# Performance work log

Hardware: AMD Instinct MI355X
Metric: run time of the kernel (lower is better)

Reference implementation:

```python
import jax, jax.numpy as jnp
import numpy as np

B, N, D = 4, 2048, 1024
H = 16
HD = D // H          # 64
SCALE = 1.0 / HD     # module uses 1/head_dim (NOT 1/sqrt)
NEG = -10000.0       # masked_fill value used by the module
THETA = 10000.0


def setup_inputs() -> dict:
    key = jax.random.key(0)
    ks = jax.random.split(key, 6)
    s = (1.0 / D) ** 0.5  # init_method_normal((1/dim)**0.5)
    return {
        "x": jax.random.normal(ks[0], (B, N, D), jnp.float32),
        "Wq": jax.random.normal(ks[1], (D, D), jnp.float32) * s,
        "Wk": jax.random.normal(ks[2], (D, D), jnp.float32) * s,
        "Wv": jax.random.normal(ks[3], (D, D), jnp.float32) * s,
        "Wo": jax.random.normal(ks[4], (D, D), jnp.float32) * s,
        "bo": jnp.zeros((D,), jnp.float32),
    }


def _rope(t):
    # t: [b, h, n, d]; interleaved-pair rotary (lucidrains rotate_queries_or_keys)
    d, n = t.shape[-1], t.shape[-2]
    inv_freq = 1.0 / (THETA ** (jnp.arange(0, d, 2, dtype=jnp.float32) / d))  # [d/2]
    ang = jnp.arange(n, dtype=jnp.float32)[:, None] * inv_freq[None, :]        # [n, d/2]
    cos = jnp.repeat(jnp.cos(ang), 2, axis=-1)  # [n, d]
    sin = jnp.repeat(jnp.sin(ang), 2, axis=-1)
    x1, x2 = t[..., ::2], t[..., 1::2]
    rot = jnp.stack([-x2, x1], axis=-1).reshape(t.shape)  # rotate_half
    return t * cos + rot * sin


def reference(x, Wq, Wk, Wv, Wo, bo):
    b, n, _ = x.shape
    # QKV projections (no bias; torch Linear: x @ W.T)
    q = (x @ Wq.T).reshape(b, n, H, HD).transpose(0, 2, 1, 3)  # [b,h,n,d]
    k = (x @ Wk.T).reshape(b, n, H, HD).transpose(0, 2, 1, 3)
    v = (x @ Wv.T).reshape(b, n, H, HD).transpose(0, 2, 1, 3)
    # RoPE on q, k
    q = _rope(q)
    k = _rope(k)
    # additive mask: 0 on/below diagonal, -10000 above (causal_mask=True path)
    i = jnp.arange(n)
    add_mask = jnp.where(i[:, None] >= i[None, :], 0.0, NEG).astype(x.dtype)  # [n,n]
    scores = jnp.einsum("bhqd,bhkd->bhqk", q, k) * SCALE + add_mask
    attn = jax.nn.softmax(scores, axis=-1)
    out = jnp.einsum("bhqk,bhkd->bhqd", attn, v)            # [b,h,n,d]
    out = out.transpose(0, 2, 1, 3).reshape(b, n, H * HD)    # [b,n,D]
    return out @ Wo.T + bo
```

## Files before the change

kernel.cpp:

```cpp
#include <hip/hip_runtime.h>
#include <hip/hip_bf16.h>
#include <math.h>

#define B_ 4
#define N_ 2048
#define D_ 1024
#define H_ 16
#define HD_ 64
#define SCALE_ 0.015625f
#define MD_ ((size_t)B_ * N_ * D_)
#define DD_ ((size_t)D_ * D_)
#define BHSZ_ ((size_t)N_ * HD_)
#define QSC_ 0.0225421143f

typedef __hip_bfloat16 bf16;
typedef __attribute__((ext_vector_type(8))) __bf16 bf16x8;
typedef __attribute__((ext_vector_type(4))) float f32x4;
typedef __attribute__((ext_vector_type(16))) float f32x16;

__device__ __forceinline__ float b2f(bf16 x) { return __bfloat162float(x); }
__device__ __forceinline__ bf16 f2b(float x) { return __float2bfloat16(x); }

__device__ __forceinline__ unsigned int pk2(float a, float b) {
  union { bf16 h[2]; unsigned int u; } t;
  t.h[0] = f2b(a); t.h[1] = f2b(b);
  return t.u;
}
__device__ __forceinline__ unsigned int pk2t(float a, float b) {
  return (__float_as_uint(a) >> 16) | (__float_as_uint(b) & 0xffff0000u);
}

__device__ __forceinline__ void gl_lds16(const bf16* g, bf16* l) {
  __builtin_amdgcn_global_load_lds(
      (const __attribute__((address_space(1))) void*)g,
      (__attribute__((address_space(3))) void*)l, 16, 0, 0);
}

__global__ __launch_bounds__(256) void cvt_all(
    const float* __restrict__ x,  const float* __restrict__ wq,
    const float* __restrict__ wk, const float* __restrict__ wv,
    const float* __restrict__ wo, bf16* __restrict__ xb,
    bf16* __restrict__ wb, float2* __restrict__ rt)
{
  const int blk = blockIdx.x;
  if (blk >= 6144) {
    const float LN_THETA = 9.210340371976184f;
    int e = ((blk - 6144) * 256 + (int)threadIdx.x) * 4;
    float fn = (float)(e >> 5);
#pragma unroll
    for (int p = 0; p < 4; ++p) {
      int i = (e & 31) + p;
      float inv = __expf(-((float)(2 * i) / (float)HD_) * LN_THETA);
      float sv, cv;
      sincosf(fn * inv, &sv, &cv);
      rt[e + p] = make_float2(cv, sv);
    }
    return;
  }
  const float* s; bf16* d; int i;
  if (blk < 4096)      { s = x;  d = xb;           i = blk; }
  else if (blk < 4608) { s = wq; d = wb;           i = blk - 4096; }
  else if (blk < 5120) { s = wk; d = wb + DD_;     i = blk - 4608; }
  else if (blk < 5632) { s = wv; d = wb + 2 * DD_; i = blk - 5120; }
  else                 { s = wo; d = wb + 3 * DD_; i = blk - 5632; }
  int e = (i * 256 + threadIdx.x) * 8;
  float4 a = *reinterpret_cast<const float4*>(s + e);
  float4 b = *reinterpret_cast<const float4*>(s + e + 4);
  bf16 t[8] = {f2b(a.x), f2b(a.y), f2b(a.z), f2b(a.w),
               f2b(b.x), f2b(b.y), f2b(b.z), f2b(b.w)};
  *reinterpret_cast<int4*>(d + e) = *reinterpret_cast<const int4*>(t);
}

template <int MODE>
__global__ __launch_bounds__(256) void mgemm(
    const bf16* __restrict__ A, const bf16* __restrict__ W,
    const float* __restrict__ bias, void* __restrict__ Cv,
    const float2* __restrict__ rt, int M, int N, int K)
{
  __shared__ bf16 As[128 * 32];
  __shared__ bf16 Ws[128 * 32];

  const int tid  = threadIdx.x;
  const int w    = tid >> 6;
  const int lane = tid & 63;
  const int bm   = blockIdx.y * 128;
  const int bn   = blockIdx.x * 128;

  const int wr = (w >> 1) * 64;
  const int wc = (w & 1) * 64;
  const int lm   = lane & 15;
  const int quad = lane >> 4;

  const int srow = lane >> 2;
  const int sslot = (lane & 3) ^ ((lane >> 3) & 3);
  const int scol = sslot * 8;

  const int rsw  = (quad ^ ((lm >> 1) & 3)) * 8;

  f32x4 acc[4][4] = {};

  for (int k0 = 0; k0 < K; k0 += 32) {
#pragma unroll
    for (int cc = 0; cc < 2; ++cc) {
      int c = w * 2 + cc;
      int r = c * 16 + srow;
      gl_lds16(A + (size_t)(bm + r) * K + k0 + scol, &As[c * 512]);
      gl_lds16(W + (size_t)(bn + r) * K + k0 + scol, &Ws[c * 512]);
    }
    __syncthreads();

    bf16x8 af[4], bf_[4];
#pragma unroll
    for (int mi = 0; mi < 4; ++mi)
      af[mi] = *reinterpret_cast<const bf16x8*>(&As[(wr + mi * 16 + lm) * 32 + rsw]);
#pragma unroll
    for (int ni = 0; ni < 4; ++ni)
      bf_[ni] = *reinterpret_cast<const bf16x8*>(&Ws[(wc + ni * 16 + lm) * 32 + rsw]);

#pragma unroll
    for (int mi = 0; mi < 4; ++mi)
#pragma unroll
      for (int ni = 0; ni < 4; ++ni)
        acc[mi][ni] = __builtin_amdgcn_mfma_f32_16x16x32_bf16(
            af[mi], bf_[ni], acc[mi][ni], 0, 0, 0);
    __syncthreads();
  }

#pragma unroll
  for (int mi = 0; mi < 4; ++mi) {
#pragma unroll
    for (int r = 0; r < 4; ++r) {
      int row = bm + wr + mi * 16 + quad * 4 + r;
#pragma unroll
      for (int ni = 0; ni < 4; ++ni) {
        int col = bn + wc + ni * 16 + lm;
        float v = acc[mi][ni][r];
        if (MODE == 1) {
          v += bias[col];
          reinterpret_cast<float*>(Cv)[(size_t)row * N + col] = v;
        } else {
          int reg = col >> 10;
          int cc  = col & 1023;
          int bb  = row >> 11;
          int n   = row & (N_ - 1);
          int hh  = cc >> 6;
          int dd  = cc & 63;
          float po = __shfl_xor(v, 1);
          if (reg < 2) {
            float2 cs = rt[(n << 5) + (dd >> 1)];
            v = (dd & 1) ? (v * cs.x + po * cs.y)
                         : (v * cs.x - po * cs.y);
            if (reg == 0) v *= QSC_;
            int t32 = n >> 5, m = n & 31;
            int s = dd >> 4, hb = (dd >> 3) & 1, j = dd & 7;
            reinterpret_cast<bf16*>(Cv)[(size_t)reg * MD_ +
                (size_t)(bb * H_ + hh) * BHSZ_ +
                (size_t)t32 * 2048 + s * 512 + hb * 256 + m * 8 + j] = f2b(v);
          } else {
            int t32 = n >> 5, kk = n & 31;
            int hf = kk >> 4, hb = (kk >> 3) & 1, j = kk & 7;
            reinterpret_cast<bf16*>(Cv)[2 * MD_ +
                (size_t)(bb * H_ + hh) * BHSZ_ +
                (size_t)t32 * 2048 + hf * 1024 + hb * 512 + dd * 8 + j] = f2b(v);
          }
        }
      }
    }
  }
}

__global__ __launch_bounds__(128) void fattn4_kernel(
    const bf16* __restrict__ Qf, const bf16* __restrict__ Kf,
    const bf16* __restrict__ Vf, bf16* __restrict__ O)
{
  __shared__ float Ls[32 * 64];
  __shared__ float Ll[64];

  const int wv   = threadIdx.x >> 6;
  const int lane = threadIdx.x & 63;
  const int blk  = blockIdx.x;
  const int xcd  = blk & 7;
  const int j    = blk >> 3;
  const int qt   = 63 - (j >> 3);
  const int bh   = xcd * 8 + (j & 7);
  const int b    = bh >> 4;
  const int h    = bh & 15;
  const int col  = lane & 31;
  const int hi   = lane >> 5;

  const bf16* Qb = Qf + (size_t)bh * BHSZ_ + (size_t)qt * 2048 + hi * 256 + col * 8;
  const bf16* Kb = Kf + (size_t)bh * BHSZ_ + hi * 256 + col * 8;
  const bf16* Vb = Vf + (size_t)bh * BHSZ_ + hi * 512 + col * 8;

  bf16x8 qb[4];
#pragma unroll
  for (int s = 0; s < 4; ++s)
    qb[s] = *reinterpret_cast<const bf16x8*>(Qb + s * 512);

  f32x16 o0 = {}, o1 = {};
  float lsum = 0.f;

  for (int kst = wv; kst <= qt; kst += 2) {
    const bf16* kp = Kb + (size_t)kst * 2048;
    f32x16 st = {};
#pragma unroll
    for (int s = 0; s < 4; ++s) {
      bf16x8 ka = *reinterpret_cast<const bf16x8*>(kp + s * 512);
      st = __builtin_amdgcn_mfma_f32_32x32x16_bf16(ka, qb[s], st, 0, 0, 0);
    }

    float pe[16];
    if (kst == qt) {
#pragma unroll
      for (int r = 0; r < 16; ++r) {
        int koff = (r & 3) + 8 * (r >> 2) + 4 * hi;
        float e = (koff <= col) ? exp2f(st[r]) : 0.f;
        pe[r] = e; lsum += e;
      }
    } else {
#pragma unroll
      for (int r = 0; r < 16; ++r) {
        float e = exp2f(st[r]);
        pe[r] = e; lsum += e;
      }
    }

    const bf16* vp = Vb + (size_t)kst * 2048;
#pragma unroll
    for (int hf = 0; hf < 2; ++hf) {
      unsigned int a0 = pk2t(pe[8 * hf + 0], pe[8 * hf + 1]);
      unsigned int a1 = pk2t(pe[8 * hf + 2], pe[8 * hf + 3]);
      unsigned int b0 = pk2t(pe[8 * hf + 4], pe[8 * hf + 5]);
      unsigned int b1 = pk2t(pe[8 * hf + 6], pe[8 * hf + 7]);
      unsigned int s0 = hi ? a0 : b0;
      unsigned int s1 = hi ? a1 : b1;
      unsigned int r0 = (unsigned int)__shfl_xor((int)s0, 32);
      unsigned int r1 = (unsigned int)__shfl_xor((int)s1, 32);
      union { uint4 u; bf16x8 v; } pb;
      pb.u.x = hi ? r0 : a0;
      pb.u.y = hi ? r1 : a1;
      pb.u.z = hi ? b0 : r0;
      pb.u.w = hi ? b1 : r1;

      bf16x8 v0 = *reinterpret_cast<const bf16x8*>(vp + hf * 1024);
      bf16x8 v1 = *reinterpret_cast<const bf16x8*>(vp + hf * 1024 + 256);
      o0 = __builtin_amdgcn_mfma_f32_32x32x16_bf16(v0, pb.v, o0, 0, 0, 0);
      o1 = __builtin_amdgcn_mfma_f32_32x32x16_bf16(v1, pb.v, o1, 0, 0, 0);
    }
  }

  if (wv == 1) {
#pragma unroll
    for (int r = 0; r < 16; ++r) {
      Ls[r * 64 + lane]        = o0[r];
      Ls[(16 + r) * 64 + lane] = o1[r];
    }
    Ll[lane] = lsum;
  }
  __syncthreads();
  if (wv == 0) {
    float lt = lsum + Ll[lane];
    lt += __shfl_xor(lt, 32);
    float inv = 1.f / lt;
#pragma unroll
    for (int r = 0; r < 16; ++r) {
      o0[r] = (o0[r] + Ls[r * 64 + lane]) * inv;
      o1[r] = (o1[r] + Ls[(16 + r) * 64 + lane]) * inv;
    }
    bf16* Op = O + ((size_t)(b * N_ + 32 * qt + col)) * D_ + h * HD_;
#pragma unroll
    for (int g = 0; g < 4; ++g) {
      uint2 u;
      u.x = pk2(o0[4 * g + 0], o0[4 * g + 1]);
      u.y = pk2(o0[4 * g + 2], o0[4 * g + 3]);
      *reinterpret_cast<uint2*>(Op + 8 * g + 4 * hi) = u;
      u.x = pk2(o1[4 * g + 0], o1[4 * g + 1]);
      u.y = pk2(o1[4 * g + 2], o1[4 * g + 3]);
      *reinterpret_cast<uint2*>(Op + 32 + 8 * g + 4 * hi) = u;
    }
  }
}

extern "C" void kernel_launch(void* const* d_in, const int* in_sizes, int n_in,
                              void* d_out, int out_size, void* d_ws, size_t ws_size,
                              hipStream_t stream)
{
  const float* x  = (const float*)d_in[0];
  const float* Wq = (const float*)d_in[1];
  const float* Wk = (const float*)d_in[2];
  const float* Wv = (const float*)d_in[3];
  const float* Wo = (const float*)d_in[4];
  const float* bo = (const float*)d_in[5];
  float* out = (float*)d_out;

  const int M = B_ * N_;

  bf16* xb  = (bf16*)d_ws;
  bf16* qf  = xb + MD_;
  bf16* kf  = qf + MD_;
  bf16* vf  = kf + MD_;
  bf16* Wqb = vf + MD_;
  bf16* Wob = Wqb + 3 * DD_;
  float2* rt = (float2*)(Wqb + 4 * DD_);
  bf16* ao  = xb;

  cvt_all<<<6208, 256, 0, stream>>>(x, Wq, Wk, Wv, Wo, xb, Wqb, rt);

  mgemm<0><<<dim3(24, 64), 256, 0, stream>>>(xb, Wqb, nullptr, qf, rt, M, 3 * D_, D_);

  fattn4_kernel<<<4096, 128, 0, stream>>>(qf, kf, vf, ao);

  mgemm<1><<<dim3(8, 64), 256, 0, stream>>>(ao, Wob, bo, out, nullptr, M, D_, D_);
}
```

Before: 277.3 us.

## Replace QKV GEMM with 256x256-tile, 8-wave, double-buffered pipelined kernel

The fused QKV projection moves to a new kernel using 256x256 output tiles, 512 threads and a double-buffered LDS pipeline. Global-to-LDS loads for future k-steps are interleaved with MFMA phases using explicit barriers, waitcnt and setprio. Blocks are remapped so neighbouring tiles land on the same XCD, which should improve cache reuse. The aim is to hide load latency and cut LDS traffic per FLOP, at the cost of much higher register and LDS pressure and fragile hand-tuned waitcnt counts.

```diff
diff --git a/kernel.cpp b/kernel.cpp
--- a/kernel.cpp
+++ b/kernel.cpp
@@ -35,6 +35,14 @@
       (const __attribute__((address_space(1))) void*)g,
       (__attribute__((address_space(3))) void*)l, 16, 0, 0);
 }
+
+__device__ __forceinline__ void fbar() {
+  asm volatile("" ::: "memory");
+  __builtin_amdgcn_s_barrier();
+  asm volatile("" ::: "memory");
+}
+
+#define MFMA16(a, b, c) __builtin_amdgcn_mfma_f32_16x16x32_bf16((a), (b), (c), 0, 0, 0)
 
 __global__ __launch_bounds__(256) void cvt_all(
     const float* __restrict__ x,  const float* __restrict__ wq,
@@ -71,11 +79,152 @@
   *reinterpret_cast<int4*>(d + e) = *reinterpret_cast<const int4*>(t);
 }
 
-template <int MODE>
-__global__ __launch_bounds__(256) void mgemm(
+__global__ __launch_bounds__(512, 2) void qkv8(
     const bf16* __restrict__ A, const bf16* __restrict__ W,
-    const float* __restrict__ bias, void* __restrict__ Cv,
-    const float2* __restrict__ rt, int M, int N, int K)
+    bf16* __restrict__ Cv, const float2* __restrict__ rt)
+{
+  __shared__ bf16 As[2 * 2 * 16 * 512];
+  __shared__ bf16 Bs[2 * 2 * 16 * 512];
+
+  const int tid  = threadIdx.x;
+  const int w    = tid >> 6;
+  const int lane = tid & 63;
+  const int wm   = w >> 2;
+  const int wn   = w & 3;
+  const int lm   = lane & 15;
+  const int quad = lane >> 4;
+
+  const int wgid = (blockIdx.x & 7) * 48 + ((int)blockIdx.x >> 3);
+  const int bn   = (wgid % 12) * 256;
+  const int bm   = (wgid / 12) * 256;
+
+  const int srow = lane >> 2;
+  const int scol = ((lane & 3) ^ ((lane >> 3) & 3)) * 8;
+  const int rsw  = (quad ^ ((lm >> 1) & 3)) * 8;
+
+  const int K = 1024;
+
+  f32x4 acc[8][4] = {};
+
+  auto stA = [&](int T, int ks) {
+    bf16* dst = &As[((T & 1) * 2 + ks) * 8192];
+    size_t kc = (size_t)T * 64 + ks * 32 + scol;
+#pragma unroll
+    for (int j = 0; j < 2; ++j) {
+      int c = 2 * w + j;
+      gl_lds16(A + (size_t)(bm + c * 16 + srow) * K + kc, dst + c * 512);
+    }
+  };
+  auto stB = [&](int T, int ks) {
+    bf16* dst = &Bs[((T & 1) * 2 + ks) * 8192];
+    size_t kc = (size_t)T * 64 + ks * 32 + scol;
+#pragma unroll
+    for (int j = 0; j < 2; ++j) {
+      int c = 2 * w + j;
+      gl_lds16(W + (size_t)(bn + c * 16 + srow) * K + kc, dst + c * 512);
+    }
+  };
+
+  auto rdA1 = [&](int T, int ks, int mi) -> bf16x8 {
+    return *reinterpret_cast<const bf16x8*>(
+        &As[(((T & 1) * 2 + ks) * 16 + wm * 8 + mi) * 512 + lm * 32 + rsw]);
+  };
+  auto rdB1 = [&](int T, int ks, int ni) -> bf16x8 {
+    return *reinterpret_cast<const bf16x8*>(
+        &Bs[(((T & 1) * 2 + ks) * 16 + wn * 4 + ni) * 512 + lm * 32 + rsw]);
+  };
+
+  bf16x8 bb[4];
+
+#define PHASE(T, KS, MH, RB, STAGE_STMT, WN) do {                             \
+    bf16x8 af_[4];                                                            \
+    _Pragma("unroll") for (int i_ = 0; i_ < 4; ++i_)                          \
+      af_[i_] = rdA1((T), (KS), (MH) * 4 + i_);                               \
+    if (RB) { _Pragma("unroll") for (int i_ = 0; i_ < 4; ++i_)                \
+      bb[i_] = rdB1((T), (KS), i_); }                                         \
+    STAGE_STMT;                                                               \
+    fbar();                                                                   \
+    asm volatile("s_waitcnt lgkmcnt(0)" ::: "memory");                        \
+    __builtin_amdgcn_s_setprio(1);                                            \
+    _Pragma("unroll") for (int i_ = 0; i_ < 4; ++i_)                          \
+      _Pragma("unroll") for (int n_ = 0; n_ < 4; ++n_)                        \
+        acc[(MH) * 4 + i_][n_] = MFMA16(af_[i_], bb[n_], acc[(MH) * 4 + i_][n_]); \
+    __builtin_amdgcn_s_setprio(0);                                            \
+    if ((WN) == 4) asm volatile("s_waitcnt vmcnt(4)" ::: "memory");           \
+    if ((WN) == 0) asm volatile("s_waitcnt vmcnt(0)" ::: "memory");           \
+    fbar();                                                                   \
+  } while (0)
+
+  stA(0, 0); stB(0, 0); stA(0, 1); stB(0, 1);
+  stA(1, 0); stB(1, 0);
+  asm volatile("s_waitcnt vmcnt(4)" ::: "memory");
+  fbar();
+
+  for (int t = 0; t < 14; t += 2) {
+    PHASE(t,     0, 0, 1, { stA(t + 1, 1); }, -1);
+    PHASE(t,     0, 1, 0, { stB(t + 1, 1); }, -1);
+    PHASE(t,     1, 0, 1, { stA(t + 2, 0); }, -1);
+    PHASE(t,     1, 1, 0, { stB(t + 2, 0); },  4);
+    PHASE(t + 1, 0, 0, 1, { stA(t + 2, 1); }, -1);
+    PHASE(t + 1, 0, 1, 0, { stB(t + 2, 1); }, -1);
+    PHASE(t + 1, 1, 0, 1, { stA(t + 3, 0); }, -1);
+    PHASE(t + 1, 1, 1, 0, { stB(t + 3, 0); },  4);
+  }
+  {
+    const int t = 14;
+    PHASE(t,     0, 0, 1, { stA(t + 1, 1); }, -1);
+    PHASE(t,     0, 1, 0, { stB(t + 1, 1); }, -1);
+    PHASE(t,     1, 0, 1, { ; },              -1);
+    PHASE(t,     1, 1, 0, { ; },               0);
+    PHASE(t + 1, 0, 0, 1, { ; },              -1);
+    PHASE(t + 1, 0, 1, 0, { ; },              -1);
+    PHASE(t + 1, 1, 0, 1, { ; },              -1);
+    PHASE(t + 1, 1, 1, 0, { ; },              -1);
+  }
+#undef PHASE
+
+#pragma unroll
+  for (int mi = 0; mi < 8; ++mi) {
+#pragma unroll
+    for (int r = 0; r < 4; ++r) {
+      int row = bm + wm * 128 + mi * 16 + quad * 4 + r;
+#pragma unroll
+      for (int ni = 0; ni < 4; ++ni) {
+        int col = bn + wn * 64 + ni * 16 + lm;
+        float v = acc[mi][ni][r];
+        int reg = col >> 10;
+        int cc  = col & 1023;
+        int bb2 = row >> 11;
+        int n   = row & (N_ - 1);
+        int hh  = cc >> 6;
+        int dd  = cc & 63;
+        float po = __shfl_xor(v, 1);
+        if (reg < 2) {
+          float2 cs = rt[(n << 5) + (dd >> 1)];
+          v = (dd & 1) ? (v * cs.x + po * cs.y)
+                       : (v * cs.x - po * cs.y);
+          if (reg == 0) v *= QSC_;
+          int t32 = n >> 5, m = n & 31;
+          int s = dd >> 4, hb = (dd >> 3) & 1, j = dd & 7;
+          Cv[(size_t)reg * MD_ +
+             (size_t)(bb2 * H_ + hh) * BHSZ_ +
+             (size_t)t32 * 2048 + s * 512 + hb * 256 + m * 8 + j] = f2b(v);
+        } else {
+          int t32 = n >> 5, kk = n & 31;
+          int hf = kk >> 4, hb = (kk >> 3) & 1, j = kk & 7;
+          Cv[2 * MD_ +
+             (size_t)(bb2 * H_ + hh) * BHSZ_ +
+             (size_t)t32 * 2048 + hf * 1024 + hb * 512 + dd * 8 + j] = f2b(v);
+        }
+      }
+    }
+  }
+}
+
+__global__ __launch_bounds__(256) void pgemm(
+    const bf16* __restrict__ A, const bf16* __restrict__ W,
+    const float* __restrict__ bias, float* __restrict__ C,
+    int M, int N, int K)
 {
   __shared__ bf16 As[128 * 32];
   __shared__ bf16 Ws[128 * 32];
@@ -94,7 +243,6 @@
   const int srow = lane >> 2;
   const int sslot = (lane & 3) ^ ((lane >> 3) & 3);
   const int scol = sslot * 8;
-
   const int rsw  = (quad ^ ((lm >> 1) & 3)) * 8;
 
   f32x4 acc[4][4] = {};
@@ -134,36 +282,7 @@
 #pragma unroll
       for (int ni = 0; ni < 4; ++ni) {
         int col = bn + wc + ni * 16 + lm;
-        float v = acc[mi][ni][r];
-        if (MODE == 1) {
-          v += bias[col];
-          reinterpret_cast<float*>(Cv)[(size_t)row * N + col] = v;
-        } else {
-          int reg = col >> 10;
-          int cc  = col & 1023;
-          int bb  = row >> 11;
-          int n   = row & (N_ - 1);
-          int hh  = cc >> 6;
-          int dd  = cc & 63;
-          float po = __shfl_xor(v, 1);
-          if (reg < 2) {
-            float2 cs = rt[(n << 5) + (dd >> 1)];
-            v = (dd & 1) ? (v * cs.x + po * cs.y)
-                         : (v * cs.x - po * cs.y);
-            if (reg == 0) v *= QSC_;
-            int t32 = n >> 5, m = n & 31;
-            int s = dd >> 4, hb = (dd >> 3) & 1, j = dd & 7;
-            reinterpret_cast<bf16*>(Cv)[(size_t)reg * MD_ +
-                (size_t)(bb * H_ + hh) * BHSZ_ +
-                (size_t)t32 * 2048 + s * 512 + hb * 256 + m * 8 + j] = f2b(v);
-          } else {
-            int t32 = n >> 5, kk = n & 31;
-            int hf = kk >> 4, hb = (kk >> 3) & 1, j = kk & 7;
-            reinterpret_cast<bf16*>(Cv)[2 * MD_ +
-                (size_t)(bb * H_ + hh) * BHSZ_ +
-                (size_t)t32 * 2048 + hf * 1024 + hb * 512 + dd * 8 + j] = f2b(v);
-          }
-        }
+        C[(size_t)row * N + col] = acc[mi][ni][r] + bias[col];
       }
     }
   }
@@ -306,9 +425,9 @@
 
   cvt_all<<<6208, 256, 0, stream>>>(x, Wq, Wk, Wv, Wo, xb, Wqb, rt);
 
-  mgemm<0><<<dim3(24, 64), 256, 0, stream>>>(xb, Wqb, nullptr, qf, rt, M, 3 * D_, D_);
+  qkv8<<<384, 512, 0, stream>>>(xb, Wqb, qf, rt);
 
   fattn4_kernel<<<4096, 128, 0, stream>>>(qf, kf, vf, ao);
 
-  mgemm<1><<<dim3(8, 64), 256, 0, stream>>>(ao, Wob, bo, out, nullptr, M, D_, D_);
-}
+  pgemm<<<dim3(8, 64), 256, 0, stream>>>(ao, Wob, bo, out, M, D_, D_);
+}
```

Measured after the change: 300.1 us. 8.2% more time.
